# Performance work log

Hardware: AMD Instinct MI355X
Metric: run time of the kernel (lower is better)

Reference implementation:

```python
import jax, jax.numpy as jnp
import numpy as np

N = 50000
E = 800000
D = 128
K_LAYER = 3
ALPHA = 0.1


def setup_inputs() -> dict:
    key = jax.random.key(0)
    ks = jax.random.split(key, 10)
    return {
        "h": jax.random.normal(ks[0], (N, D), dtype=jnp.float32),
        "src0": jax.random.randint(ks[1], (E,), 0, N),
        "dst0": jax.random.randint(ks[2], (E,), 0, N),
        "src1": jax.random.randint(ks[3], (E,), 0, N),
        "dst1": jax.random.randint(ks[4], (E,), 0, N),
        "W_h": jax.random.normal(ks[5], (D, D), dtype=jnp.float32) * 0.02,
        "b_h": jnp.zeros((D,), dtype=jnp.float32),
        "W_att": jax.random.normal(ks[6], (D, D), dtype=jnp.float32) * 0.02,
        "b_att": jnp.zeros((D,), dtype=jnp.float32),
        "q_att": jax.random.normal(ks[7], (D,), dtype=jnp.float32) * 0.02,
    }


def _appnp(feat, src, dst):
    # DGL APPNPConv with symmetric degree normalization, eval mode (no edge drop)
    ones = jnp.ones((src.shape[0],), dtype=feat.dtype)
    deg_out = jax.ops.segment_sum(ones, src, num_segments=N)
    deg_in = jax.ops.segment_sum(ones, dst, num_segments=N)
    norm_s = jnp.clip(deg_out, 1.0, None) ** -0.5  # [N]
    norm_d = jnp.clip(deg_in, 1.0, None) ** -0.5   # [N]
    h0 = feat

    def step(x, _):
        m = (x * norm_s[:, None])[src]                       # [E, D] gather
        agg = jax.ops.segment_sum(m, dst, num_segments=N)    # [N, D] scatter-add
        x = (1.0 - ALPHA) * agg * norm_d[:, None] + ALPHA * h0
        return x, None

    x, _ = jax.lax.scan(step, feat, None, length=K_LAYER)
    return x


def reference(h, src0, dst0, src1, dst1, W_h, b_h, W_att, b_att, q_att):
    # per-ntype Linear + ReLU
    h = jax.nn.relu(h @ W_h + b_h)
    # APPNP propagation per metapath graph
    z = jnp.stack([_appnp(h, src0, dst0), _appnp(h, src1, dst1)])  # [P, N, D]
    # semantic attention: mean over nodes of q . tanh(z W + b)
    w = jnp.mean(jnp.tanh(z @ W_att + b_att) @ q_att, axis=1)  # [P]
    beta = jax.nn.softmax(w)
    return jnp.einsum("p,pnd->nd", beta, z)
```

## Files before the change

### kernel.cpp

```cpp
#include <hip/hip_runtime.h>

#define NN 50000
#define EE 800000
#define DD 128
#define NCHUNK 32
#define CH (EE / NCHUNK)
#define NRANGE 4
#define RSIZE (NN / NRANGE)
#define NSB 49
#define NSTRIP (NN / 16)

typedef __attribute__((ext_vector_type(8))) short bf16x8;
typedef __attribute__((ext_vector_type(4))) float f32x4;

__device__ __forceinline__ unsigned short f2b(float x) {
    unsigned u = __float_as_uint(x);
    unsigned r = (u + 0x7fffu + ((u >> 16) & 1u)) >> 16;
    return (unsigned short)r;
}
__device__ __forceinline__ float b2f_lo(unsigned w) {
    return __uint_as_float((w & 0xffffu) << 16);
}
__device__ __forceinline__ float b2f_hi(unsigned w) {
    return __uint_as_float(w & 0xffff0000u);
}

__global__ __launch_bounds__(256) void k_prep(
    const float* __restrict__ Wh, const float* __restrict__ Wa,
    short* __restrict__ WTh, short* __restrict__ WTa)
{
    const float* W = blockIdx.x ? Wa : Wh;
    short* WT      = blockIdx.x ? WTa : WTh;
    for (int i = threadIdx.x; i < DD * DD; i += 256) {
        int n = i >> 7, k = i & 127;
        WT[i] = (short)f2b(W[k * DD + n]);
    }
}

__global__ __launch_bounds__(256) void k_linear_mfma(
    const float* __restrict__ h, const short* __restrict__ WT,
    const float* __restrict__ b, unsigned short* __restrict__ out)
{
    __shared__ char ldsb[32768];
    int tid = threadIdx.x;
    for (int i = tid; i < DD * DD / 8; i += 256) {
        int n = i >> 4, k8 = i & 15;
        int4 v = ((const int4*)WT)[i];
        *(int4*)(ldsb + n * 256 + ((k8 * 16) ^ ((n & 7) << 4))) = v;
    }
    __syncthreads();
    int wid = tid >> 6, l = tid & 63;
    int s = blockIdx.x * 4 + wid;
    if (s >= NSTRIP) return;
    int lr = l & 15, lg = l >> 4;
    int row0 = s * 16;
    const float4* ap = (const float4*)(h + (size_t)(row0 + lr) * DD + lg * 8);
    bf16x8 a[4];
    #pragma unroll 4
    for (int t = 0; t < 4; ++t) {
        float4 f0 = ap[8 * t], f1 = ap[8 * t + 1];
        a[t][0] = f2b(f0.x); a[t][1] = f2b(f0.y); a[t][2] = f2b(f0.z); a[t][3] = f2b(f0.w);
        a[t][4] = f2b(f1.x); a[t][5] = f2b(f1.y); a[t][6] = f2b(f1.z); a[t][7] = f2b(f1.w);
    }
    f32x4 acc[8];
    #pragma unroll 8
    for (int c = 0; c < 8; ++c) acc[c] = (f32x4){0.f, 0.f, 0.f, 0.f};
    #pragma unroll 8
    for (int c = 0; c < 8; ++c) {
        int n = c * 16 + lr;
        #pragma unroll 4
        for (int t = 0; t < 4; ++t) {
            bf16x8 bv = *(bf16x8*)(ldsb + n * 256 + ((t * 64 + lg * 16) ^ ((n & 7) << 4)));
            acc[c] = __builtin_amdgcn_mfma_f32_16x16x32_bf16(a[t], bv, acc[c], 0, 0, 0);
        }
    }
    #pragma unroll 8
    for (int c = 0; c < 8; ++c) {
        int col = c * 16 + lr;
        float bc = b[col];
        #pragma unroll 4
        for (int r = 0; r < 4; ++r) {
            float v = acc[c][r] + bc;
            out[(size_t)(row0 + lg * 4 + r) * DD + col] = f2b(fmaxf(v, 0.f));
        }
    }
}

__global__ __launch_bounds__(256) void k_attn_mfma(
    const float* __restrict__ z0, const float* __restrict__ z1,
    const short* __restrict__ WT, const float* __restrict__ b,
    const float* __restrict__ q, float* __restrict__ S)
{
    __shared__ char ldsb[32768];
    __shared__ float red[4];
    const float* z = blockIdx.y ? z1 : z0;
    int tid = threadIdx.x;
    for (int i = tid; i < DD * DD / 8; i += 256) {
        int n = i >> 4, k8 = i & 15;
        int4 v = ((const int4*)WT)[i];
        *(int4*)(ldsb + n * 256 + ((k8 * 16) ^ ((n & 7) << 4))) = v;
    }
    __syncthreads();
    int wid = tid >> 6, l = tid & 63;
    int s = blockIdx.x * 4 + wid;
    float part = 0.f;
    if (s < NSTRIP) {
        int lr = l & 15, lg = l >> 4;
        int row0 = s * 16;
        const float4* ap = (const float4*)(z + (size_t)(row0 + lr) * DD + lg * 8);
        bf16x8 a[4];
        #pragma unroll 4
        for (int t = 0; t < 4; ++t) {
            float4 f0 = ap[8 * t], f1 = ap[8 * t + 1];
            a[t][0] = f2b(f0.x); a[t][1] = f2b(f0.y); a[t][2] = f2b(f0.z); a[t][3] = f2b(f0.w);
            a[t][4] = f2b(f1.x); a[t][5] = f2b(f1.y); a[t][6] = f2b(f1.z); a[t][7] = f2b(f1.w);
        }
        f32x4 acc[8];
        #pragma unroll 8
        for (int c = 0; c < 8; ++c) acc[c] = (f32x4){0.f, 0.f, 0.f, 0.f};
        #pragma unroll 8
        for (int c = 0; c < 8; ++c) {
            int n = c * 16 + lr;
            #pragma unroll 4
            for (int t = 0; t < 4; ++t) {
                bf16x8 bv = *(bf16x8*)(ldsb + n * 256 + ((t * 64 + lg * 16) ^ ((n & 7) << 4)));
                acc[c] = __builtin_amdgcn_mfma_f32_16x16x32_bf16(a[t], bv, acc[c], 0, 0, 0);
            }
        }
        #pragma unroll 8
        for (int c = 0; c < 8; ++c) {
            int col = c * 16 + lr;
            float bc = b[col], qc = q[col];
            #pragma unroll 4
            for (int r = 0; r < 4; ++r)
                part += tanhf(acc[c][r] + bc) * qc;
        }
    }
    for (int sh = 32; sh > 0; sh >>= 1)
        part += __shfl_down(part, sh);
    if (l == 0) red[wid] = part;
    __syncthreads();
    if (tid == 0)
        atomicAdd(&S[blockIdx.y], red[0] + red[1] + red[2] + red[3]);
}

__global__ __launch_bounds__(256) void k_hist(
    const int* __restrict__ s0, const int* __restrict__ d0,
    const int* __restrict__ s1, const int* __restrict__ d1,
    int* __restrict__ partial)
{
    __shared__ int hist[RSIZE];
    int c = blockIdx.x, rg = blockIdx.y, a = blockIdx.z;
    const int* idx = (a == 0) ? s0 : (a == 1) ? d0 : (a == 2) ? s1 : d1;
    int lo = rg * RSIZE;
    for (int i = threadIdx.x; i < RSIZE; i += 256) hist[i] = 0;
    __syncthreads();
    int beg = c * CH, end = beg + CH;
    for (int i = beg + threadIdx.x; i < end; i += 256) {
        int v = idx[i] - lo;
        if ((unsigned)v < (unsigned)RSIZE) atomicAdd(&hist[v], 1);
    }
    __syncthreads();
    int* dst = partial + ((size_t)a * NCHUNK + c) * NN + lo;
    for (int i = threadIdx.x; i < RSIZE; i += 256) dst[i] = hist[i];
}

__global__ __launch_bounds__(256) void k_reduce(
    int* __restrict__ partial,
    float* ns0, float* nd0, float* ns1, float* nd1,
    int* cdeg0, int* cdeg1)
{
    int n = blockIdx.x * 256 + threadIdx.x;
    int a = blockIdx.y;
    if (n >= NN) return;
    int run = 0;
    bool isdst = a & 1;
    for (int c = 0; c < NCHUNK; ++c) {
        size_t ix = ((size_t)a * NCHUNK + c) * NN + n;
        int t = partial[ix];
        if (isdst) partial[ix] = run;
        run += t;
    }
    float nv = rsqrtf((float)(run > 1 ? run : 1));
    if (a == 0) ns0[n] = nv;
    else if (a == 1) { nd0[n] = nv; cdeg0[n] = run; }
    else if (a == 2) ns1[n] = nv;
    else { nd1[n] = nv; cdeg1[n] = run; }
}

__global__ __launch_bounds__(256) void k_scan1(
    const int* __restrict__ cdeg0, const int* __restrict__ cdeg1,
    int* __restrict__ bsum)
{
    const int* dg = blockIdx.y ? cdeg1 : cdeg0;
    __shared__ int ws_[4];
    int tid = threadIdx.x;
    int n0 = blockIdx.x * 1024 + tid * 4;
    int s = 0;
    #pragma unroll
    for (int k = 0; k < 4; ++k) {
        int n = n0 + k;
        if (n < NN) s += dg[n];
    }
    for (int sh = 32; sh > 0; sh >>= 1) s += __shfl_down(s, sh);
    if ((tid & 63) == 0) ws_[tid >> 6] = s;
    __syncthreads();
    if (tid == 0)
        bsum[blockIdx.y * NSB + blockIdx.x] = ws_[0] + ws_[1] + ws_[2] + ws_[3];
}

__global__ __launch_bounds__(64) void k_scan2(
    const int* __restrict__ bsum, int* __restrict__ bbase,
    int* off0, int* off1)
{
    int p = threadIdx.x;
    if (p < 2) {
        int run = 0;
        for (int b = 0; b < NSB; ++b) {
            bbase[p * NSB + b] = run;
            run += bsum[p * NSB + b];
        }
        (p ? off1 : off0)[NN] = run;
    }
}

__global__ __launch_bounds__(256) void k_scan3(
    const int* __restrict__ cdeg0, const int* __restrict__ cdeg1,
    const int* __restrict__ bbase, int* off0, int* off1)
{
    const int* dg = blockIdx.y ? cdeg1 : cdeg0;
    int* off      = blockIdx.y ? off1  : off0;
    __shared__ int ts[256];
    int tid = threadIdx.x;
    int n0 = blockIdx.x * 1024 + tid * 4;
    int d0 = 0, d1 = 0, d2 = 0, d3 = 0;
    if (n0 + 0 < NN) d0 = dg[n0 + 0];
    if (n0 + 1 < NN) d1 = dg[n0 + 1];
    if (n0 + 2 < NN) d2 = dg[n0 + 2];
    if (n0 + 3 < NN) d3 = dg[n0 + 3];
    int tot = d0 + d1 + d2 + d3;
    ts[tid] = tot;
    __syncthreads();
    for (int s = 1; s < 256; s <<= 1) {
        int u = (tid >= s) ? ts[tid - s] : 0;
        __syncthreads();
        ts[tid] += u;
        __syncthreads();
    }
    int base = bbase[blockIdx.y * NSB + blockIdx.x] + ts[tid] - tot;
    if (n0 + 0 < NN) off[n0 + 0] = base;
    if (n0 + 1 < NN) off[n0 + 1] = base + d0;
    if (n0 + 2 < NN) off[n0 + 2] = base + d0 + d1;
    if (n0 + 3 < NN) off[n0 + 3] = base + d0 + d1 + d2;
}

__global__ __launch_bounds__(256) void k_fill2(
    const int* __restrict__ src0, const int* __restrict__ dst0,
    const int* __restrict__ src1, const int* __restrict__ dst1,
    const int* __restrict__ partial,
    const int* __restrict__ off0, const int* __restrict__ off1,
    int* __restrict__ es0, int* __restrict__ es1)
{
    __shared__ int cur[RSIZE];
    int c = blockIdx.x, rg = blockIdx.y, p = blockIdx.z;
    const int* src = p ? src1 : src0;
    const int* dst = p ? dst1 : dst0;
    const int* off = p ? off1 : off0;
    int* es        = p ? es1  : es0;
    const int* pfx = partial + ((size_t)(1 + 2 * p) * NCHUNK + c) * NN;
    int lo = rg * RSIZE;
    for (int i = threadIdx.x; i < RSIZE; i += 256) cur[i] = 0;
    __syncthreads();
    int beg = c * CH, end = beg + CH;
    for (int i = beg + threadIdx.x; i < end; i += 256) {
        int d = dst[i];
        int v = d - lo;
        if ((unsigned)v < (unsigned)RSIZE) {
            int s = src[i];
            int r = atomicAdd(&cur[v], 1);
            es[off[d] + pfx[d] + r] = s;
        }
    }
}

template<int OUTF32>
__global__ __launch_bounds__(256) void k_appnp3(
    const unsigned* __restrict__ xin0, const unsigned* __restrict__ xin1,
    void* __restrict__ xo0, void* __restrict__ xo1,
    const unsigned* __restrict__ h0,
    const int* __restrict__ off0, const int* __restrict__ es0,
    const float* __restrict__ ns0, const float* __restrict__ nd0,
    const int* __restrict__ off1, const int* __restrict__ es1,
    const float* __restrict__ ns1, const float* __restrict__ nd1)
{
    int bid = blockIdx.x;
    int xcd = bid & 7;
    int p = xcd >> 2;
    int pblk = (bid >> 3) * 4 + (xcd & 3);
    const unsigned* xin = p ? xin1 : xin0;
    const int* off = p ? off1 : off0;
    const int* es  = p ? es1  : es0;
    const float* ns = p ? ns1 : ns0;
    const float* nd = p ? nd1 : nd0;
    int wid = pblk * 4 + (threadIdx.x >> 6);
    int l = threadIdx.x & 63;
    int g = l >> 4, f = l & 15;
    int v = wid;
    int beg = off[v], end = off[v + 1];
    const uint4* xin4 = (const uint4*)xin;
    float acc[8];
    #pragma unroll
    for (int i = 0; i < 8; ++i) acc[i] = 0.f;
    for (int e = beg; e < end; e += 8) {
        int e0 = e + g, e1 = e + 4 + g;
        bool p0 = e0 < end, p1 = e1 < end;
        int u0 = p0 ? es[e0] : 0;
        int u1 = p1 ? es[e1] : 0;
        float s0 = p0 ? ns[u0] : 0.f;
        float s1 = p1 ? ns[u1] : 0.f;
        uint4 w0 = xin4[(size_t)u0 * 16 + f];
        uint4 w1 = xin4[(size_t)u1 * 16 + f];
        acc[0] = fmaf(b2f_lo(w0.x), s0, acc[0]);
        acc[1] = fmaf(b2f_hi(w0.x), s0, acc[1]);
        acc[2] = fmaf(b2f_lo(w0.y), s0, acc[2]);
        acc[3] = fmaf(b2f_hi(w0.y), s0, acc[3]);
        acc[4] = fmaf(b2f_lo(w0.z), s0, acc[4]);
        acc[5] = fmaf(b2f_hi(w0.z), s0, acc[5]);
        acc[6] = fmaf(b2f_lo(w0.w), s0, acc[6]);
        acc[7] = fmaf(b2f_hi(w0.w), s0, acc[7]);
        acc[0] = fmaf(b2f_lo(w1.x), s1, acc[0]);
        acc[1] = fmaf(b2f_hi(w1.x), s1, acc[1]);
        acc[2] = fmaf(b2f_lo(w1.y), s1, acc[2]);
        acc[3] = fmaf(b2f_hi(w1.y), s1, acc[3]);
        acc[4] = fmaf(b2f_lo(w1.z), s1, acc[4]);
        acc[5] = fmaf(b2f_hi(w1.z), s1, acc[5]);
        acc[6] = fmaf(b2f_lo(w1.w), s1, acc[6]);
        acc[7] = fmaf(b2f_hi(w1.w), s1, acc[7]);
    }
    #pragma unroll
    for (int i = 0; i < 8; ++i) {
        acc[i] += __shfl_xor(acc[i], 16);
        acc[i] += __shfl_xor(acc[i], 32);
    }
    if (g == 0) {
        float scale = 0.9f * nd[v];
        uint4 hw = ((const uint4*)h0)[(size_t)v * 16 + f];
        float r0 = fmaf(acc[0], scale, 0.1f * b2f_lo(hw.x));
        float r1 = fmaf(acc[1], scale, 0.1f * b2f_hi(hw.x));
        float r2 = fmaf(acc[2], scale, 0.1f * b2f_lo(hw.y));
        float r3 = fmaf(acc[3], scale, 0.1f * b2f_hi(hw.y));
        float r4 = fmaf(acc[4], scale, 0.1f * b2f_lo(hw.z));
        float r5 = fmaf(acc[5], scale, 0.1f * b2f_hi(hw.z));
        float r6 = fmaf(acc[6], scale, 0.1f * b2f_lo(hw.w));
        float r7 = fmaf(acc[7], scale, 0.1f * b2f_hi(hw.w));
        if (OUTF32) {
            float4* xo = (float4*)(p ? xo1 : xo0);
            xo[(size_t)v * 32 + f * 2]     = make_float4(r0, r1, r2, r3);
            xo[(size_t)v * 32 + f * 2 + 1] = make_float4(r4, r5, r6, r7);
        } else {
            uint4* xo = (uint4*)(p ? xo1 : xo0);
            uint4 ov;
            ov.x = (unsigned)f2b(r0) | ((unsigned)f2b(r1) << 16);
            ov.y = (unsigned)f2b(r2) | ((unsigned)f2b(r3) << 16);
            ov.z = (unsigned)f2b(r4) | ((unsigned)f2b(r5) << 16);
            ov.w = (unsigned)f2b(r6) | ((unsigned)f2b(r7) << 16);
            xo[(size_t)v * 16 + f] = ov;
        }
    }
}

__global__ __launch_bounds__(256) void k_combine(
    const float* __restrict__ z0, const float* __restrict__ z1,
    const float* __restrict__ S, float* __restrict__ out)
{
    float w0 = S[0] * (1.0f / NN);
    float w1 = S[1] * (1.0f / NN);
    float m  = fmaxf(w0, w1);
    float e0 = expf(w0 - m), e1 = expf(w1 - m);
    float inv = 1.0f / (e0 + e1);
    float b0 = e0 * inv, b1 = e1 * inv;
    const float4* a = (const float4*)z0;
    const float4* c = (const float4*)z1;
    float4* o = (float4*)out;
    int i = blockIdx.x * 256 + threadIdx.x;
    int stride = gridDim.x * 256;
    for (; i < NN * DD / 4; i += stride) {
        float4 x = a[i], y = c[i];
        float4 r;
        r.x = b0 * x.x + b1 * y.x;
        r.y = b0 * x.y + b1 * y.y;
        r.z = b0 * x.z + b1 * y.z;
        r.w = b0 * x.w + b1 * y.w;
        o[i] = r;
    }
}

extern "C" void kernel_launch(void* const* d_in, const int* in_sizes, int n_in,
                              void* d_out, int out_size, void* d_ws, size_t ws_size,
                              hipStream_t stream)
{
    const float* h     = (const float*)d_in[0];
    const int*   src0  = (const int*)d_in[1];
    const int*   dst0  = (const int*)d_in[2];
    const int*   src1  = (const int*)d_in[3];
    const int*   dst1  = (const int*)d_in[4];
    const float* W_h   = (const float*)d_in[5];
    const float* b_h   = (const float*)d_in[6];
    const float* W_att = (const float*)d_in[7];
    const float* b_att = (const float*)d_in[8];
    const float* q_att = (const float*)d_in[9];
    float* out = (float*)d_out;

    char* ws = (char*)d_ws;
    size_t o = 0;
    auto alloc = [&](size_t bytes) -> void* {
        void* p = ws + o;
        o += (bytes + 255) & ~(size_t)255;
        return p;
    };
    const size_t ND  = (size_t)NN * DD * sizeof(float);
    const size_t NDb = (size_t)NN * DD * sizeof(short);
    unsigned short* h1b = (unsigned short*)alloc(NDb);
    int*   partial = (int*)alloc((size_t)4 * NCHUNK * NN * sizeof(int));
    unsigned* A0 = (unsigned*)partial;
    unsigned* A1 = A0 + (size_t)NN * DD / 2;
    float* z0 = (float*)alloc(ND);
    float* z1 = (float*)alloc(ND);
    unsigned* B0 = (unsigned*)alloc(NDb);
    unsigned* B1 = (unsigned*)alloc(NDb);
    float* ns0 = (float*)alloc(NN * 4);
    float* nd0 = (float*)alloc(NN * 4);
    float* ns1 = (float*)alloc(NN * 4);
    float* nd1 = (float*)alloc(NN * 4);
    int* cdeg0 = (int*)alloc(NN * 4);
    int* cdeg1 = (int*)alloc(NN * 4);
    int* off0 = (int*)alloc((NN + 1) * 4);
    int* off1 = (int*)alloc((NN + 1) * 4);
    int* es0  = (int*)alloc(EE * 4);
    int* es1  = (int*)alloc(EE * 4);
    int* bsum  = (int*)alloc(2 * NSB * 4);
    int* bbase = (int*)alloc(2 * NSB * 4);
    short* WTh = (short*)alloc(DD * DD * 2);
    short* WTa = (short*)alloc(DD * DD * 2);
    float* S   = (float*)alloc(256);
    hipMemsetAsync(S, 0, 256, stream);

    k_prep<<<2, 256, 0, stream>>>(W_h, W_att, WTh, WTa);
    k_linear_mfma<<<(NSTRIP + 3) / 4, 256, 0, stream>>>(h, WTh, b_h, h1b);
    k_hist<<<dim3(NCHUNK, NRANGE, 4), 256, 0, stream>>>(src0, dst0, src1, dst1, partial);
    k_reduce<<<dim3((NN + 255) / 256, 4), 256, 0, stream>>>(
        partial, ns0, nd0, ns1, nd1, cdeg0, cdeg1);
    k_scan1<<<dim3(NSB, 2), 256, 0, stream>>>(cdeg0, cdeg1, bsum);
    k_scan2<<<1, 64, 0, stream>>>(bsum, bbase, off0, off1);
    k_scan3<<<dim3(NSB, 2), 256, 0, stream>>>(cdeg0, cdeg1, bbase, off0, off1);
    k_fill2<<<dim3(NCHUNK, NRANGE, 2), 256, 0, stream>>>(
        src0, dst0, src1, dst1, partial, off0, off1, es0, es1);
    const unsigned* h1u = (const unsigned*)h1b;
    const int agrid = 2 * ((NN + 3) / 4);
    k_appnp3<0><<<agrid, 256, 0, stream>>>(
        h1u, h1u, A0, A1, h1u,
        off0, es0, ns0, nd0, off1, es1, ns1, nd1);
    k_appnp3<0><<<agrid, 256, 0, stream>>>(
        A0, A1, B0, B1, h1u,
        off0, es0, ns0, nd0, off1, es1, ns1, nd1);
    k_appnp3<1><<<agrid, 256, 0, stream>>>(
        B0, B1, z0, z1, h1u,
        off0, es0, ns0, nd0, off1, es1, ns1, nd1);
    k_attn_mfma<<<dim3((NSTRIP + 3) / 4, 2), 256, 0, stream>>>(
        z0, z1, WTa, b_att, q_att, S);
    k_combine<<<2048, 256, 0, stream>>>(z0, z1, S, out);
    (void)in_sizes; (void)n_in; (void)out_size; (void)ws_size;
}
```

Baseline: 462.1 us.

## Pack degree histograms and CSR edge indices into 16-bit storage

Per-chunk histograms and prefix counts are now stored as 16-bit values, packed two per 32-bit shared-memory word, which halves LDS use and lets the node-range split drop from four to two with 512-thread blocks. CSR source indices shrink to unsigned short, which cuts index traffic in the three propagation passes and in the fill kernel. The ping-pong buffers A0/A1 no longer alias the partial array and get their own allocations. Storing node ids as 16-bit truncates them, because N is 50000 and fits in an unsigned short only since 50000 < 65536. Per-chunk counts also have to stay under 65536.

```diff
diff --git a/kernel.cpp b/kernel.cpp
--- a/kernel.cpp
+++ b/kernel.cpp
@@ -5,7 +5,7 @@
 #define DD 128
 #define NCHUNK 32
 #define CH (EE / NCHUNK)
-#define NRANGE 4
+#define NRANGE 2
 #define RSIZE (NN / NRANGE)
 #define NSB 49
 #define NSTRIP (NN / 16)
@@ -144,29 +144,30 @@
         atomicAdd(&S[blockIdx.y], red[0] + red[1] + red[2] + red[3]);
 }
 
-__global__ __launch_bounds__(256) void k_hist(
+__global__ __launch_bounds__(512) void k_hist(
     const int* __restrict__ s0, const int* __restrict__ d0,
     const int* __restrict__ s1, const int* __restrict__ d1,
-    int* __restrict__ partial)
-{
-    __shared__ int hist[RSIZE];
+    unsigned short* __restrict__ partial)
+{
+    __shared__ unsigned h2[RSIZE / 2];
     int c = blockIdx.x, rg = blockIdx.y, a = blockIdx.z;
     const int* idx = (a == 0) ? s0 : (a == 1) ? d0 : (a == 2) ? s1 : d1;
     int lo = rg * RSIZE;
-    for (int i = threadIdx.x; i < RSIZE; i += 256) hist[i] = 0;
+    for (int i = threadIdx.x; i < RSIZE / 2; i += 512) h2[i] = 0;
     __syncthreads();
     int beg = c * CH, end = beg + CH;
-    for (int i = beg + threadIdx.x; i < end; i += 256) {
+    for (int i = beg + threadIdx.x; i < end; i += 512) {
         int v = idx[i] - lo;
-        if ((unsigned)v < (unsigned)RSIZE) atomicAdd(&hist[v], 1);
-    }
-    __syncthreads();
-    int* dst = partial + ((size_t)a * NCHUNK + c) * NN + lo;
-    for (int i = threadIdx.x; i < RSIZE; i += 256) dst[i] = hist[i];
+        if ((unsigned)v < (unsigned)RSIZE)
+            atomicAdd(&h2[v >> 1], (v & 1) ? 0x10000u : 1u);
+    }
+    __syncthreads();
+    unsigned* dst = (unsigned*)(partial + ((size_t)a * NCHUNK + c) * NN + lo);
+    for (int i = threadIdx.x; i < RSIZE / 2; i += 512) dst[i] = h2[i];
 }
 
 __global__ __launch_bounds__(256) void k_reduce(
-    int* __restrict__ partial,
+    unsigned short* __restrict__ partial,
     float* ns0, float* nd0, float* ns1, float* nd1,
     int* cdeg0, int* cdeg1)
 {
@@ -178,7 +179,7 @@
     for (int c = 0; c < NCHUNK; ++c) {
         size_t ix = ((size_t)a * NCHUNK + c) * NN + n;
         int t = partial[ix];
-        if (isdst) partial[ix] = run;
+        if (isdst) partial[ix] = (unsigned short)run;
         run += t;
     }
     float nv = rsqrtf((float)(run > 1 ? run : 1));
@@ -254,31 +255,32 @@
     if (n0 + 3 < NN) off[n0 + 3] = base + d0 + d1 + d2;
 }
 
-__global__ __launch_bounds__(256) void k_fill2(
+__global__ __launch_bounds__(512) void k_fill2(
     const int* __restrict__ src0, const int* __restrict__ dst0,
     const int* __restrict__ src1, const int* __restrict__ dst1,
-    const int* __restrict__ partial,
+    const unsigned short* __restrict__ partial,
     const int* __restrict__ off0, const int* __restrict__ off1,
-    int* __restrict__ es0, int* __restrict__ es1)
-{
-    __shared__ int cur[RSIZE];
+    unsigned short* __restrict__ es0, unsigned short* __restrict__ es1)
+{
+    __shared__ unsigned cur2[RSIZE / 2];
     int c = blockIdx.x, rg = blockIdx.y, p = blockIdx.z;
     const int* src = p ? src1 : src0;
     const int* dst = p ? dst1 : dst0;
     const int* off = p ? off1 : off0;
-    int* es        = p ? es1  : es0;
-    const int* pfx = partial + ((size_t)(1 + 2 * p) * NCHUNK + c) * NN;
+    unsigned short* es = p ? es1 : es0;
+    const unsigned short* pfx = partial + ((size_t)(1 + 2 * p) * NCHUNK + c) * NN;
     int lo = rg * RSIZE;
-    for (int i = threadIdx.x; i < RSIZE; i += 256) cur[i] = 0;
+    for (int i = threadIdx.x; i < RSIZE / 2; i += 512) cur2[i] = 0;
     __syncthreads();
     int beg = c * CH, end = beg + CH;
-    for (int i = beg + threadIdx.x; i < end; i += 256) {
+    for (int i = beg + threadIdx.x; i < end; i += 512) {
         int d = dst[i];
         int v = d - lo;
         if ((unsigned)v < (unsigned)RSIZE) {
             int s = src[i];
-            int r = atomicAdd(&cur[v], 1);
-            es[off[d] + pfx[d] + r] = s;
+            unsigned old = atomicAdd(&cur2[v >> 1], (v & 1) ? 0x10000u : 1u);
+            int r = (v & 1) ? (int)(old >> 16) : (int)(old & 0xffffu);
+            es[off[d] + (int)pfx[d] + r] = (unsigned short)s;
         }
     }
 }
@@ -288,9 +290,9 @@
     const unsigned* __restrict__ xin0, const unsigned* __restrict__ xin1,
     void* __restrict__ xo0, void* __restrict__ xo1,
     const unsigned* __restrict__ h0,
-    const int* __restrict__ off0, const int* __restrict__ es0,
+    const int* __restrict__ off0, const unsigned short* __restrict__ es0,
     const float* __restrict__ ns0, const float* __restrict__ nd0,
-    const int* __restrict__ off1, const int* __restrict__ es1,
+    const int* __restrict__ off1, const unsigned short* __restrict__ es1,
     const float* __restrict__ ns1, const float* __restrict__ nd1)
 {
     int bid = blockIdx.x;
@@ -299,7 +301,7 @@
     int pblk = (bid >> 3) * 4 + (xcd & 3);
     const unsigned* xin = p ? xin1 : xin0;
     const int* off = p ? off1 : off0;
-    const int* es  = p ? es1  : es0;
+    const unsigned short* es = p ? es1 : es0;
     const float* ns = p ? ns1 : ns0;
     const float* nd = p ? nd1 : nd0;
     int wid = pblk * 4 + (threadIdx.x >> 6);
@@ -314,8 +316,8 @@
     for (int e = beg; e < end; e += 8) {
         int e0 = e + g, e1 = e + 4 + g;
         bool p0 = e0 < end, p1 = e1 < end;
-        int u0 = p0 ? es[e0] : 0;
-        int u1 = p1 ? es[e1] : 0;
+        int u0 = p0 ? (int)es[e0] : 0;
+        int u1 = p1 ? (int)es[e1] : 0;
         float s0 = p0 ? ns[u0] : 0.f;
         float s1 = p1 ? ns[u1] : 0.f;
         uint4 w0 = xin4[(size_t)u0 * 16 + f];
@@ -421,13 +423,14 @@
     const size_t ND  = (size_t)NN * DD * sizeof(float);
     const size_t NDb = (size_t)NN * DD * sizeof(short);
     unsigned short* h1b = (unsigned short*)alloc(NDb);
-    int*   partial = (int*)alloc((size_t)4 * NCHUNK * NN * sizeof(int));
-    unsigned* A0 = (unsigned*)partial;
-    unsigned* A1 = A0 + (size_t)NN * DD / 2;
+    unsigned short* partial =
+        (unsigned short*)alloc((size_t)4 * NCHUNK * NN * sizeof(short));
+    unsigned* A0 = (unsigned*)alloc(NDb);
+    unsigned* A1 = (unsigned*)alloc(NDb);
+    unsigned* B0 = (unsigned*)alloc(NDb);
+    unsigned* B1 = (unsigned*)alloc(NDb);
     float* z0 = (float*)alloc(ND);
     float* z1 = (float*)alloc(ND);
-    unsigned* B0 = (unsigned*)alloc(NDb);
-    unsigned* B1 = (unsigned*)alloc(NDb);
     float* ns0 = (float*)alloc(NN * 4);
     float* nd0 = (float*)alloc(NN * 4);
     float* ns1 = (float*)alloc(NN * 4);
@@ -436,8 +439,8 @@
     int* cdeg1 = (int*)alloc(NN * 4);
     int* off0 = (int*)alloc((NN + 1) * 4);
     int* off1 = (int*)alloc((NN + 1) * 4);
-    int* es0  = (int*)alloc(EE * 4);
-    int* es1  = (int*)alloc(EE * 4);
+    unsigned short* es0 = (unsigned short*)alloc(EE * 2);
+    unsigned short* es1 = (unsigned short*)alloc(EE * 2);
     int* bsum  = (int*)alloc(2 * NSB * 4);
     int* bbase = (int*)alloc(2 * NSB * 4);
     short* WTh = (short*)alloc(DD * DD * 2);
@@ -447,13 +450,13 @@
 
     k_prep<<<2, 256, 0, stream>>>(W_h, W_att, WTh, WTa);
     k_linear_mfma<<<(NSTRIP + 3) / 4, 256, 0, stream>>>(h, WTh, b_h, h1b);
-    k_hist<<<dim3(NCHUNK, NRANGE, 4), 256, 0, stream>>>(src0, dst0, src1, dst1, partial);
+    k_hist<<<dim3(NCHUNK, NRANGE, 4), 512, 0, stream>>>(src0, dst0, src1, dst1, partial);
     k_reduce<<<dim3((NN + 255) / 256, 4), 256, 0, stream>>>(
         partial, ns0, nd0, ns1, nd1, cdeg0, cdeg1);
     k_scan1<<<dim3(NSB, 2), 256, 0, stream>>>(cdeg0, cdeg1, bsum);
     k_scan2<<<1, 64, 0, stream>>>(bsum, bbase, off0, off1);
     k_scan3<<<dim3(NSB, 2), 256, 0, stream>>>(cdeg0, cdeg1, bbase, off0, off1);
-    k_fill2<<<dim3(NCHUNK, NRANGE, 2), 256, 0, stream>>>(
+    k_fill2<<<dim3(NCHUNK, NRANGE, 2), 512, 0, stream>>>(
         src0, dst0, src1, dst1, partial, off0, off1, es0, es1);
     const unsigned* h1u = (const unsigned*)h1b;
     const int agrid = 2 * ((NN + 3) / 4);
```

Measured after the change: 430.4 us. 6.9% less time.
